# Kernel tuning notes

Hardware: AMD Instinct MI355X
Metric: run time of the kernel (lower is better)

Reference implementation:

```python
import jax, jax.numpy as jnp
import numpy as np

N = 100000
E = 1600000
D_IN = 64
D_H = 64
D_OUT = 10
G = 512
EPS = 1e-5


def setup_inputs() -> dict:
    key = jax.random.key(0)
    ks = jax.random.split(key, 12)
    x = jax.random.normal(ks[0], (N, D_IN), dtype=jnp.float32)
    edge_index = jax.random.randint(ks[1], (2, E), 0, N, dtype=jnp.int64)
    batch = jnp.sort(jax.random.randint(ks[2], (N,), 0, G, dtype=jnp.int64))

    def glorot(k, fan_in, fan_out):
        lim = float(np.sqrt(6.0 / (fan_in + fan_out)))
        return jax.random.uniform(k, (fan_in, fan_out), jnp.float32, -lim, lim)

    params = {
        'W1': glorot(ks[3], D_IN, D_H), 'b1': jnp.zeros((D_H,), jnp.float32),
        'g1': jnp.ones((D_H,), jnp.float32), 'be1': jnp.zeros((D_H,), jnp.float32),
        'W2': glorot(ks[4], D_H, D_H), 'b2': jnp.zeros((D_H,), jnp.float32),
        'g2': jnp.ones((D_H,), jnp.float32), 'be2': jnp.zeros((D_H,), jnp.float32),
        'W3': glorot(ks[5], D_H, D_H), 'b3': jnp.zeros((D_H,), jnp.float32),
        'g3': jnp.ones((D_H,), jnp.float32), 'be3': jnp.zeros((D_H,), jnp.float32),
        'Wfc': glorot(ks[6], D_H, D_OUT), 'bfc': jnp.zeros((D_OUT,), jnp.float32),
    }
    return dict(x=x, edge_index=edge_index, batch=batch, **params)


def _gcn_prep(edge_index):
    # add self-loops, compute symmetric degree normalization (PyG GCNConv)
    loop = jnp.arange(N, dtype=edge_index.dtype)
    src = jnp.concatenate([edge_index[0], loop])  # [E+N]
    dst = jnp.concatenate([edge_index[1], loop])
    deg = jax.ops.segment_sum(jnp.ones_like(dst, dtype=jnp.float32), dst, num_segments=N)
    dinv = jnp.where(deg > 0, jax.lax.rsqrt(deg), 0.0)
    norm = dinv[src] * dinv[dst]  # [E+N]
    return src, dst, norm


def _gcn_conv(x, src, dst, norm, W, b):
    h = x @ W                                   # [N, D]
    msg = h[src] * norm[:, None]                # gather + scale [E+N, D]
    out = jax.ops.segment_sum(msg, dst, num_segments=N)  # scatter-add
    return out + b


def _bn_relu(x, gamma, beta):
    # BatchNorm1d with batch statistics (training mode, biased variance)
    mu = jnp.mean(x, axis=0)
    var = jnp.mean(jnp.square(x - mu), axis=0)
    y = (x - mu) * jax.lax.rsqrt(var + EPS) * gamma + beta
    return jax.nn.relu(y)


def reference(x, edge_index, batch, W1, b1, g1, be1, W2, b2, g2, be2,
              W3, b3, g3, be3, Wfc, bfc):
    src, dst, norm = _gcn_prep(edge_index)
    # dropout treated as identity (eval-mode) for deterministic reference
    h = _bn_relu(_gcn_conv(x, src, dst, norm, W1, b1), g1, be1)
    h = _bn_relu(_gcn_conv(h, src, dst, norm, W2, b2), g2, be2)
    h = _bn_relu(_gcn_conv(h, src, dst, norm, W3, b3), g3, be3)
    # global mean pool over graphs
    sums = jax.ops.segment_sum(h, batch, num_segments=G)       # [G, D]
    cnt = jax.ops.segment_sum(jnp.ones((N,), jnp.float32), batch, num_segments=G)
    pooled = sums / jnp.maximum(cnt, 1.0)[:, None]
    return pooled @ Wfc + bfc  # [G, D_OUT]
```

## Files before the change

kernel.cpp:

```cpp
#include <hip/hip_runtime.h>

#define NNODES 100000
#define NEDGES 1600000
#define DH 64
#define NG 512
#define DOUT 10
#define EPSV 1e-5f
#define SCAN_BLKS 391
#define PCH 128

typedef short bf16x8 __attribute__((ext_vector_type(8)));
typedef float f32x4 __attribute__((ext_vector_type(4)));

__device__ inline unsigned bf16_rne(float x) {
    unsigned u = __float_as_uint(x);
    return (u + 0x7fffu + ((u >> 16) & 1u)) >> 16;
}
__device__ inline float bflo(unsigned u) { return __uint_as_float(u << 16); }
__device__ inline float bfhi(unsigned u) { return __uint_as_float(u & 0xffff0000u); }

__global__ void k_zero(int* __restrict__ cntdeg, float* __restrict__ pooled,
                       int* __restrict__ gstart, int* __restrict__ gend,
                       float* __restrict__ stats) {
    int i = blockIdx.x * 256 + threadIdx.x;
    if (i < NNODES) cntdeg[i] = 0;
    if (i < NG * DH) pooled[i] = 0.0f;
    if (i < NG) { gstart[i] = 0; gend[i] = 0; }
    if (i < 384) stats[i] = 0.0f;
}

__global__ void k_count(const int* __restrict__ dstE, int* __restrict__ cntdeg) {
    int e2 = blockIdx.x * 256 + threadIdx.x;
    if (e2 * 2 + 1 < NEDGES) {
        int2 d = ((const int2*)dstE)[e2];
        atomicAdd(&cntdeg[d.x], 1);
        atomicAdd(&cntdeg[d.y], 1);
    } else if (e2 * 2 < NEDGES) {
        atomicAdd(&cntdeg[dstE[e2 * 2]], 1);
    }
}

__global__ void k_scan1(const int* __restrict__ cntdeg, int* __restrict__ bsum,
                        float* __restrict__ dinv, const int* __restrict__ batch,
                        int* __restrict__ gstart, int* __restrict__ gend) {
    __shared__ int ls[256];
    int t = threadIdx.x, i = blockIdx.x * 256 + t;
    int v = (i < NNODES) ? cntdeg[i] : 0;
    if (i < NNODES) {
        dinv[i] = rsqrtf(1.0f + (float)v);
        int g = batch[i];
        if (i == 0 || batch[i - 1] != g) gstart[g] = i;
        if (i == NNODES - 1 || batch[i + 1] != g) gend[g] = i + 1;
    }
    ls[t] = v;
    __syncthreads();
#pragma unroll
    for (int off = 128; off > 0; off >>= 1) {
        if (t < off) ls[t] += ls[t + off];
        __syncthreads();
    }
    if (t == 0) bsum[blockIdx.x] = ls[0];
}

__global__ void __launch_bounds__(512) k_scan2(const int* __restrict__ bsum,
                                               int* __restrict__ boff) {
    __shared__ int ps[512];
    int t = threadIdx.x;
    int v = (t < SCAN_BLKS) ? bsum[t] : 0;
    ps[t] = v;
    __syncthreads();
#pragma unroll
    for (int off = 1; off < 512; off <<= 1) {
        int u = (t >= off) ? ps[t - off] : 0;
        __syncthreads();
        ps[t] += u;
        __syncthreads();
    }
    if (t < SCAN_BLKS) boff[t] = ps[t] - v;
}

__global__ void k_scan3(const int* __restrict__ cntdeg, const int* __restrict__ boff,
                        int* __restrict__ rowptr, int* __restrict__ cursor) {
    __shared__ int ps[256];
    int t = threadIdx.x, i = blockIdx.x * 256 + t;
    int v = (i < NNODES) ? cntdeg[i] : 0;
    ps[t] = v;
    __syncthreads();
#pragma unroll
    for (int off = 1; off < 256; off <<= 1) {
        int u = (t >= off) ? ps[t - off] : 0;
        __syncthreads();
        ps[t] += u;
        __syncthreads();
    }
    if (i < NNODES) {
        int ex = boff[blockIdx.x] + ps[t] - v;
        rowptr[i] = ex;
        cursor[i] = ex;
    }
    if (i == 0) rowptr[NNODES] = NEDGES;
}

__global__ void k_fill(const int* __restrict__ srcE, const int* __restrict__ dstE,
                       const float* __restrict__ dinv, int* __restrict__ cursor,
                       int2* __restrict__ csr) {
    int e = blockIdx.x * 256 + threadIdx.x;
    if (e >= NEDGES) return;
    int s = srcE[e], d = dstE[e];
    int pos = atomicAdd(&cursor[d], 1);
    float nm = dinv[s] * dinv[d];
    csr[pos] = make_int2(s, __float_as_int(nm));
}

__global__ void k_wprep(const float* __restrict__ W0, const float* __restrict__ W1,
                        const float* __restrict__ W2, short* __restrict__ wf) {
    int t = blockIdx.x * 256 + threadIdx.x;
    if (t >= 1536) return;
    int layer = t >> 9;
    int rem = t & 511;
    int ct = rem >> 7, ks = (rem >> 6) & 1, lane = rem & 63;
    const float* W = (layer == 0) ? W0 : (layer == 1) ? W1 : W2;
    short* hi = wf + layer * 8192 + rem * 8;
    short* lo = hi + 4096;
#pragma unroll
    for (int i = 0; i < 8; ++i) {
        int k = ks * 32 + ((lane >> 4) << 3) + i;
        int n = ct * 16 + (lane & 15);
        float v = W[k * 64 + n];
        unsigned h = bf16_rne(v);
        float fh = __uint_as_float(h << 16);
        unsigned l = bf16_rne(v - fh);
        hi[i] = (short)h;
        lo[i] = (short)l;
    }
}

template <int AFFINE>
__global__ void __launch_bounds__(256) k_mgemm(const float* __restrict__ in,
        const short* __restrict__ wf, const float* __restrict__ scale,
        const float* __restrict__ shift, unsigned short* __restrict__ out) {
    const int tid = threadIdx.x;
    const int wv = tid >> 6, l = tid & 63;
    const int r0 = blockIdx.x * 64 + wv * 16;
    const int row = r0 + (l & 15);
    const int kq = (l >> 4) << 3;

    float a[2][8];
    if (row < NNODES) {
        const float* rp = in + (size_t)row * 64 + kq;
        *(float4*)&a[0][0] = *(const float4*)(rp);
        *(float4*)&a[0][4] = *(const float4*)(rp + 4);
        *(float4*)&a[1][0] = *(const float4*)(rp + 32);
        *(float4*)&a[1][4] = *(const float4*)(rp + 36);
    } else {
#pragma unroll
        for (int ks = 0; ks < 2; ++ks)
#pragma unroll
            for (int i = 0; i < 8; ++i) a[ks][i] = 0.0f;
    }
    if (AFFINE) {
#pragma unroll
        for (int ks = 0; ks < 2; ++ks) {
            float4 sc0 = *(const float4*)(scale + kq + ks * 32);
            float4 sc1 = *(const float4*)(scale + kq + ks * 32 + 4);
            float4 sh0 = *(const float4*)(shift + kq + ks * 32);
            float4 sh1 = *(const float4*)(shift + kq + ks * 32 + 4);
            a[ks][0] = fmaxf(fmaf(a[ks][0], sc0.x, sh0.x), 0.0f);
            a[ks][1] = fmaxf(fmaf(a[ks][1], sc0.y, sh0.y), 0.0f);
            a[ks][2] = fmaxf(fmaf(a[ks][2], sc0.z, sh0.z), 0.0f);
            a[ks][3] = fmaxf(fmaf(a[ks][3], sc0.w, sh0.w), 0.0f);
            a[ks][4] = fmaxf(fmaf(a[ks][4], sc1.x, sh1.x), 0.0f);
            a[ks][5] = fmaxf(fmaf(a[ks][5], sc1.y, sh1.y), 0.0f);
            a[ks][6] = fmaxf(fmaf(a[ks][6], sc1.z, sh1.z), 0.0f);
            a[ks][7] = fmaxf(fmaf(a[ks][7], sc1.w, sh1.w), 0.0f);
        }
    }

    bf16x8 ah[2], al[2];
#pragma unroll
    for (int ks = 0; ks < 2; ++ks)
#pragma unroll
        for (int i = 0; i < 8; ++i) {
            unsigned h = bf16_rne(a[ks][i]);
            float fh = __uint_as_float(h << 16);
            ah[ks][i] = (short)h;
            al[ks][i] = (short)bf16_rne(a[ks][i] - fh);
        }

    const int rb = r0 + ((l >> 4) << 2);
    const int cb = l & 15;
#pragma unroll
    for (int ct = 0; ct < 4; ++ct) {
        const short* base = wf + (ct * 128 + l) * 8;
        bf16x8 wh0 = *(const bf16x8*)(base);
        bf16x8 wh1 = *(const bf16x8*)(base + 64 * 8);
        bf16x8 wl0 = *(const bf16x8*)(base + 4096);
        bf16x8 wl1 = *(const bf16x8*)(base + 4096 + 64 * 8);
        f32x4 acc = {0.0f, 0.0f, 0.0f, 0.0f};
        acc = __builtin_amdgcn_mfma_f32_16x16x32_bf16(ah[0], wh0, acc, 0, 0, 0);
        acc = __builtin_amdgcn_mfma_f32_16x16x32_bf16(ah[1], wh1, acc, 0, 0, 0);
        acc = __builtin_amdgcn_mfma_f32_16x16x32_bf16(al[0], wh0, acc, 0, 0, 0);
        acc = __builtin_amdgcn_mfma_f32_16x16x32_bf16(al[1], wh1, acc, 0, 0, 0);
        acc = __builtin_amdgcn_mfma_f32_16x16x32_bf16(ah[0], wl0, acc, 0, 0, 0);
        acc = __builtin_amdgcn_mfma_f32_16x16x32_bf16(ah[1], wl1, acc, 0, 0, 0);
        int n = ct * 16 + cb;
#pragma unroll
        for (int r = 0; r < 4; ++r)
            if (rb + r < NNODES) out[(size_t)(rb + r) * 64 + n] = (unsigned short)bf16_rne(acc[r]);
    }
}

__global__ void k_gather(const uint4* __restrict__ h, const int2* __restrict__ csr,
                         const int* __restrict__ rowptr, const float* __restrict__ dinv,
                         const float* __restrict__ bias, float* __restrict__ agg) {
    int t = blockIdx.x * 256 + threadIdx.x;
    int i = t >> 3, q = t & 7;
    if (i >= NNODES) return;
    float dv = dinv[i];
    float sn = dv * dv;
    float4 b0 = ((const float4*)bias)[q * 2];
    float4 b1 = ((const float4*)bias)[q * 2 + 1];
    uint4 hv = h[(size_t)i * 8 + q];
    float A[8], B[8];
    A[0] = fmaf(bflo(hv.x), sn, b0.x); A[1] = fmaf(bfhi(hv.x), sn, b0.y);
    A[2] = fmaf(bflo(hv.y), sn, b0.z); A[3] = fmaf(bfhi(hv.y), sn, b0.w);
    A[4] = fmaf(bflo(hv.z), sn, b1.x); A[5] = fmaf(bfhi(hv.z), sn, b1.y);
    A[6] = fmaf(bflo(hv.w), sn, b1.z); A[7] = fmaf(bfhi(hv.w), sn, b1.w);
#pragma unroll
    for (int k = 0; k < 8; ++k) B[k] = 0.0f;

    int e0 = rowptr[i], e1 = rowptr[i + 1];
    int e = e0;
    for (; e + 4 <= e1; e += 4) {
        int2 ea = csr[e], eb = csr[e + 1], ec = csr[e + 2], ed = csr[e + 3];
        float na = __int_as_float(ea.y), nb = __int_as_float(eb.y);
        float nc = __int_as_float(ec.y), nd = __int_as_float(ed.y);
        uint4 va = h[(size_t)ea.x * 8 + q];
        uint4 vb = h[(size_t)eb.x * 8 + q];
        uint4 vc = h[(size_t)ec.x * 8 + q];
        uint4 vd = h[(size_t)ed.x * 8 + q];
        A[0] = fmaf(bflo(va.x), na, A[0]); A[1] = fmaf(bfhi(va.x), na, A[1]);
        A[2] = fmaf(bflo(va.y), na, A[2]); A[3] = fmaf(bfhi(va.y), na, A[3]);
        A[4] = fmaf(bflo(va.z), na, A[4]); A[5] = fmaf(bfhi(va.z), na, A[5]);
        A[6] = fmaf(bflo(va.w), na, A[6]); A[7] = fmaf(bfhi(va.w), na, A[7]);
        B[0] = fmaf(bflo(vb.x), nb, B[0]); B[1] = fmaf(bfhi(vb.x), nb, B[1]);
        B[2] = fmaf(bflo(vb.y), nb, B[2]); B[3] = fmaf(bfhi(vb.y), nb, B[3]);
        B[4] = fmaf(bflo(vb.z), nb, B[4]); B[5] = fmaf(bfhi(vb.z), nb, B[5]);
        B[6] = fmaf(bflo(vb.w), nb, B[6]); B[7] = fmaf(bfhi(vb.w), nb, B[7]);
        A[0] = fmaf(bflo(vc.x), nc, A[0]); A[1] = fmaf(bfhi(vc.x), nc, A[1]);
        A[2] = fmaf(bflo(vc.y), nc, A[2]); A[3] = fmaf(bfhi(vc.y), nc, A[3]);
        A[4] = fmaf(bflo(vc.z), nc, A[4]); A[5] = fmaf(bfhi(vc.z), nc, A[5]);
        A[6] = fmaf(bflo(vc.w), nc, A[6]); A[7] = fmaf(bfhi(vc.w), nc, A[7]);
        B[0] = fmaf(bflo(vd.x), nd, B[0]); B[1] = fmaf(bfhi(vd.x), nd, B[1]);
        B[2] = fmaf(bflo(vd.y), nd, B[2]); B[3] = fmaf(bfhi(vd.y), nd, B[3]);
        B[4] = fmaf(bflo(vd.z), nd, B[4]); B[5] = fmaf(bfhi(vd.z), nd, B[5]);
        B[6] = fmaf(bflo(vd.w), nd, B[6]); B[7] = fmaf(bfhi(vd.w), nd, B[7]);
    }
    for (; e + 2 <= e1; e += 2) {
        int2 ea = csr[e], eb = csr[e + 1];
        float na = __int_as_float(ea.y), nb = __int_as_float(eb.y);
        uint4 va = h[(size_t)ea.x * 8 + q];
        uint4 vb = h[(size_t)eb.x * 8 + q];
        A[0] = fmaf(bflo(va.x), na, A[0]); A[1] = fmaf(bfhi(va.x), na, A[1]);
        A[2] = fmaf(bflo(va.y), na, A[2]); A[3] = fmaf(bfhi(va.y), na, A[3]);
        A[4] = fmaf(bflo(va.z), na, A[4]); A[5] = fmaf(bfhi(va.z), na, A[5]);
        A[6] = fmaf(bflo(va.w), na, A[6]); A[7] = fmaf(bfhi(va.w), na, A[7]);
        B[0] = fmaf(bflo(vb.x), nb, B[0]); B[1] = fmaf(bfhi(vb.x), nb, B[1]);
        B[2] = fmaf(bflo(vb.y), nb, B[2]); B[3] = fmaf(bfhi(vb.y), nb, B[3]);
        B[4] = fmaf(bflo(vb.z), nb, B[4]); B[5] = fmaf(bfhi(vb.z), nb, B[5]);
        B[6] = fmaf(bflo(vb.w), nb, B[6]); B[7] = fmaf(bfhi(vb.w), nb, B[7]);
    }
    if (e < e1) {
        int2 ea = csr[e];
        float na = __int_as_float(ea.y);
        uint4 va = h[(size_t)ea.x * 8 + q];
        A[0] = fmaf(bflo(va.x), na, A[0]); A[1] = fmaf(bfhi(va.x), na, A[1]);
        A[2] = fmaf(bflo(va.y), na, A[2]); A[3] = fmaf(bfhi(va.y), na, A[3]);
        A[4] = fmaf(bflo(va.z), na, A[4]); A[5] = fmaf(bfhi(va.z), na, A[5]);
        A[6] = fmaf(bflo(va.w), na, A[6]); A[7] = fmaf(bfhi(va.w), na, A[7]);
    }
    float4 r0, r1;
    r0.x = A[0] + B[0]; r0.y = A[1] + B[1]; r0.z = A[2] + B[2]; r0.w = A[3] + B[3];
    r1.x = A[4] + B[4]; r1.y = A[5] + B[5]; r1.z = A[6] + B[6]; r1.w = A[7] + B[7];
    ((float4*)agg)[(size_t)i * 16 + q * 2] = r0;
    ((float4*)agg)[(size_t)i * 16 + q * 2 + 1] = r1;
}

__global__ void k_stats(const float* __restrict__ agg, float* __restrict__ stats) {
    const int c = threadIdx.x & 63;
    float s = 0.f, ss = 0.f;
    for (int r = blockIdx.x * 4 + (threadIdx.x >> 6); r < NNODES; r += gridDim.x * 4) {
        float v = agg[(size_t)r * 64 + c];
        s += v;
        ss = fmaf(v, v, ss);
    }
    __shared__ float ls[256], lss[256];
    ls[threadIdx.x] = s;
    lss[threadIdx.x] = ss;
    __syncthreads();
    if (threadIdx.x < 64) {
        s = ls[c] + ls[c + 64] + ls[c + 128] + ls[c + 192];
        ss = lss[c] + lss[c + 64] + lss[c + 128] + lss[c + 192];
        unsafeAtomicAdd(&stats[c], s);
        unsafeAtomicAdd(&stats[64 + c], ss);
    }
}

__global__ void k_bnparams(const float* __restrict__ stats, const float* __restrict__ g,
                           const float* __restrict__ be, float* __restrict__ scale,
                           float* __restrict__ shift) {
    int c = threadIdx.x;
    if (c < 64) {
        float mu = stats[c] * (1.0f / NNODES);
        float var = stats[64 + c] * (1.0f / NNODES) - mu * mu;
        float sc = g[c] * rsqrtf(var + EPSV);
        scale[c] = sc;
        shift[c] = fmaf(-mu, sc, be[c]);
    }
}

__global__ void k_pool(const float* __restrict__ agg, const float* __restrict__ scale,
                       const float* __restrict__ shift, const int* __restrict__ batch,
                       float* __restrict__ pooled) {
    const int tid = threadIdx.x;
    const int c = tid & 63, r = tid >> 6;
    const int i0 = blockIdx.x * PCH;
    const float sc = scale[c], sh = shift[c];
    float acc = 0.0f;
    int cur = -1;
#pragma unroll 4
    for (int k = 0; k < PCH / 4; ++k) {
        int i = i0 + k * 4 + r;
        if (i >= NNODES) break;
        int g = batch[i];
        if (g != cur) {
            if (cur >= 0) unsafeAtomicAdd(&pooled[cur * 64 + c], acc);
            acc = 0.0f;
            cur = g;
        }
        acc += fmaxf(fmaf(agg[(size_t)i * 64 + c], sc, sh), 0.0f);
    }
    if (cur >= 0) unsafeAtomicAdd(&pooled[cur * 64 + c], acc);
}

__global__ void k_final(const float* __restrict__ pooled, const int* __restrict__ gstart,
                        const int* __restrict__ gend, const float* __restrict__ Wfc,
                        const float* __restrict__ bfc, float* __restrict__ out) {
    __shared__ float p[64];
    __shared__ float ic;
    int g = blockIdx.x, tid = threadIdx.x;
    p[tid] = pooled[(size_t)g * 64 + tid];
    if (tid == 0) ic = 1.0f / fmaxf((float)(gend[g] - gstart[g]), 1.0f);
    __syncthreads();
    if (tid < DOUT) {
        float a = bfc[tid];
#pragma unroll 8
        for (int c = 0; c < 64; ++c) a = fmaf(p[c] * ic, Wfc[c * DOUT + tid], a);
        out[g * DOUT + tid] = a;
    }
}

extern "C" void kernel_launch(void* const* d_in, const int* in_sizes, int n_in,
                              void* d_out, int out_size, void* d_ws, size_t ws_size,
                              hipStream_t stream) {
    const float* x = (const float*)d_in[0];
    const int* ei = (const int*)d_in[1];
    const int* batch = (const int*)d_in[2];
    const int* srcE = ei;
    const int* dstE = ei + NEDGES;
    const float* W[3] = {(const float*)d_in[3], (const float*)d_in[7], (const float*)d_in[11]};
    const float* B[3] = {(const float*)d_in[4], (const float*)d_in[8], (const float*)d_in[12]};
    const float* Gm[3] = {(const float*)d_in[5], (const float*)d_in[9], (const float*)d_in[13]};
    const float* Be[3] = {(const float*)d_in[6], (const float*)d_in[10], (const float*)d_in[14]};
    const float* Wfc = (const float*)d_in[15];
    const float* bfc = (const float*)d_in[16];
    float* out = (float*)d_out;

    float* f = (float*)d_ws;
    float* dinv = f;
    int* cntdeg = (int*)(f + 100000);
    int* rowptr = (int*)(f + 200000);
    int* cursor = (int*)(f + 300016);
    int2* csr = (int2*)(f + 400016);
    unsigned short* h = (unsigned short*)(f + 3600016);
    float* agg = f + 3600016 + 3200000;
    float* stats = agg + (size_t)NNODES * DH;
    float* scale = stats + 384;
    float* shift = scale + 64;
    float* pooled = shift + 64;
    int* gstart = (int*)(pooled + NG * DH);
    int* gend = gstart + NG;
    short* wf = (short*)(gend + NG);
    int* bsum = (int*)((short*)wf + 24576);
    int* boff = bsum + 400;

    k_zero<<<(NNODES + 255) / 256, 256, 0, stream>>>(cntdeg, pooled, gstart, gend, stats);
    k_count<<<(NEDGES / 2 + 255) / 256, 256, 0, stream>>>(dstE, cntdeg);
    k_scan1<<<SCAN_BLKS, 256, 0, stream>>>(cntdeg, bsum, dinv, batch, gstart, gend);
    k_scan2<<<1, 512, 0, stream>>>(bsum, boff);
    k_scan3<<<SCAN_BLKS, 256, 0, stream>>>(cntdeg, boff, rowptr, cursor);
    k_fill<<<(NEDGES + 255) / 256, 256, 0, stream>>>(srcE, dstE, dinv, cursor, csr);
    k_wprep<<<6, 256, 0, stream>>>(W[0], W[1], W[2], wf);

    const int gemm_grid = (NNODES + 63) / 64;
    for (int l = 0; l < 3; ++l) {
        const float* in = (l == 0) ? x : agg;
        if (l == 0)
            k_mgemm<0><<<gemm_grid, 256, 0, stream>>>(in, wf + l * 8192, scale, shift, h);
        else
            k_mgemm<1><<<gemm_grid, 256, 0, stream>>>(in, wf + l * 8192, scale, shift, h);
        k_gather<<<(NNODES * 8 + 255) / 256, 256, 0, stream>>>((const uint4*)h, csr, rowptr, dinv, B[l], agg);
        k_stats<<<512, 256, 0, stream>>>(agg, stats + l * 128);
        k_bnparams<<<1, 64, 0, stream>>>(stats + l * 128, Gm[l], Be[l], scale, shift);
    }

    k_pool<<<(NNODES + PCH - 1) / PCH, 256, 0, stream>>>(agg, scale, shift, batch, pooled);
    k_final<<<NG, 64, 0, stream>>>(pooled, gstart, gend, Wfc, bfc, out);
}
```

Before: 549.6 us.

## Store only source indices in CSR and factor dst normalization out of gather

The CSR now holds only the 4-byte source index instead of an (index, norm) pair. The gather applies the source-side dinv through a random load of dinv[src] and multiplies the destination-side dinv once after accumulation, which halves the CSR stream bandwidth and the fill-kernel writes. The trade is an extra scattered dinv load per edge, though that 400KB array should stay cache resident. Separately, the stats kernel now reads float4 vectors, with 16 row groups per block and a wider shared-memory reduction.

```diff
diff --git a/kernel.cpp b/kernel.cpp
--- a/kernel.cpp
+++ b/kernel.cpp
@@ -102,14 +102,12 @@
 }
 
 __global__ void k_fill(const int* __restrict__ srcE, const int* __restrict__ dstE,
-                       const float* __restrict__ dinv, int* __restrict__ cursor,
-                       int2* __restrict__ csr) {
+                       int* __restrict__ cursor, int* __restrict__ csr4) {
     int e = blockIdx.x * 256 + threadIdx.x;
     if (e >= NEDGES) return;
     int s = srcE[e], d = dstE[e];
     int pos = atomicAdd(&cursor[d], 1);
-    float nm = dinv[s] * dinv[d];
-    csr[pos] = make_int2(s, __float_as_int(nm));
+    csr4[pos] = s;
 }
 
 __global__ void k_wprep(const float* __restrict__ W0, const float* __restrict__ W1,
@@ -210,35 +208,31 @@
     }
 }
 
-__global__ void k_gather(const uint4* __restrict__ h, const int2* __restrict__ csr,
+__global__ void k_gather(const uint4* __restrict__ h, const int* __restrict__ csr4,
                          const int* __restrict__ rowptr, const float* __restrict__ dinv,
                          const float* __restrict__ bias, float* __restrict__ agg) {
     int t = blockIdx.x * 256 + threadIdx.x;
     int i = t >> 3, q = t & 7;
     if (i >= NNODES) return;
     float dv = dinv[i];
-    float sn = dv * dv;
-    float4 b0 = ((const float4*)bias)[q * 2];
-    float4 b1 = ((const float4*)bias)[q * 2 + 1];
     uint4 hv = h[(size_t)i * 8 + q];
     float A[8], B[8];
-    A[0] = fmaf(bflo(hv.x), sn, b0.x); A[1] = fmaf(bfhi(hv.x), sn, b0.y);
-    A[2] = fmaf(bflo(hv.y), sn, b0.z); A[3] = fmaf(bfhi(hv.y), sn, b0.w);
-    A[4] = fmaf(bflo(hv.z), sn, b1.x); A[5] = fmaf(bfhi(hv.z), sn, b1.y);
-    A[6] = fmaf(bflo(hv.w), sn, b1.z); A[7] = fmaf(bfhi(hv.w), sn, b1.w);
+    A[0] = bflo(hv.x) * dv; A[1] = bfhi(hv.x) * dv;
+    A[2] = bflo(hv.y) * dv; A[3] = bfhi(hv.y) * dv;
+    A[4] = bflo(hv.z) * dv; A[5] = bfhi(hv.z) * dv;
+    A[6] = bflo(hv.w) * dv; A[7] = bfhi(hv.w) * dv;
 #pragma unroll
     for (int k = 0; k < 8; ++k) B[k] = 0.0f;
 
     int e0 = rowptr[i], e1 = rowptr[i + 1];
     int e = e0;
     for (; e + 4 <= e1; e += 4) {
-        int2 ea = csr[e], eb = csr[e + 1], ec = csr[e + 2], ed = csr[e + 3];
-        float na = __int_as_float(ea.y), nb = __int_as_float(eb.y);
-        float nc = __int_as_float(ec.y), nd = __int_as_float(ed.y);
-        uint4 va = h[(size_t)ea.x * 8 + q];
-        uint4 vb = h[(size_t)eb.x * 8 + q];
-        uint4 vc = h[(size_t)ec.x * 8 + q];
-        uint4 vd = h[(size_t)ed.x * 8 + q];
+        int sa = csr4[e], sb = csr4[e + 1], sc = csr4[e + 2], sd = csr4[e + 3];
+        float na = dinv[sa], nb = dinv[sb], nc = dinv[sc], nd = dinv[sd];
+        uint4 va = h[(size_t)sa * 8 + q];
+        uint4 vb = h[(size_t)sb * 8 + q];
+        uint4 vc = h[(size_t)sc * 8 + q];
+        uint4 vd = h[(size_t)sd * 8 + q];
         A[0] = fmaf(bflo(va.x), na, A[0]); A[1] = fmaf(bfhi(va.x), na, A[1]);
         A[2] = fmaf(bflo(va.y), na, A[2]); A[3] = fmaf(bfhi(va.y), na, A[3]);
         A[4] = fmaf(bflo(va.z), na, A[4]); A[5] = fmaf(bfhi(va.z), na, A[5]);
@@ -257,10 +251,10 @@
         B[6] = fmaf(bflo(vd.w), nd, B[6]); B[7] = fmaf(bfhi(vd.w), nd, B[7]);
     }
     for (; e + 2 <= e1; e += 2) {
-        int2 ea = csr[e], eb = csr[e + 1];
-        float na = __int_as_float(ea.y), nb = __int_as_float(eb.y);
-        uint4 va = h[(size_t)ea.x * 8 + q];
-        uint4 vb = h[(size_t)eb.x * 8 + q];
+        int sa = csr4[e], sb = csr4[e + 1];
+        float na = dinv[sa], nb = dinv[sb];
+        uint4 va = h[(size_t)sa * 8 + q];
+        uint4 vb = h[(size_t)sb * 8 + q];
         A[0] = fmaf(bflo(va.x), na, A[0]); A[1] = fmaf(bfhi(va.x), na, A[1]);
         A[2] = fmaf(bflo(va.y), na, A[2]); A[3] = fmaf(bfhi(va.y), na, A[3]);
         A[4] = fmaf(bflo(va.z), na, A[4]); A[5] = fmaf(bfhi(va.z), na, A[5]);
@@ -271,38 +265,52 @@
         B[6] = fmaf(bflo(vb.w), nb, B[6]); B[7] = fmaf(bfhi(vb.w), nb, B[7]);
     }
     if (e < e1) {
-        int2 ea = csr[e];
-        float na = __int_as_float(ea.y);
-        uint4 va = h[(size_t)ea.x * 8 + q];
+        int sa = csr4[e];
+        float na = dinv[sa];
+        uint4 va = h[(size_t)sa * 8 + q];
         A[0] = fmaf(bflo(va.x), na, A[0]); A[1] = fmaf(bfhi(va.x), na, A[1]);
         A[2] = fmaf(bflo(va.y), na, A[2]); A[3] = fmaf(bfhi(va.y), na, A[3]);
         A[4] = fmaf(bflo(va.z), na, A[4]); A[5] = fmaf(bfhi(va.z), na, A[5]);
         A[6] = fmaf(bflo(va.w), na, A[6]); A[7] = fmaf(bfhi(va.w), na, A[7]);
     }
+    float4 b0 = ((const float4*)bias)[q * 2];
+    float4 b1 = ((const float4*)bias)[q * 2 + 1];
     float4 r0, r1;
-    r0.x = A[0] + B[0]; r0.y = A[1] + B[1]; r0.z = A[2] + B[2]; r0.w = A[3] + B[3];
-    r1.x = A[4] + B[4]; r1.y = A[5] + B[5]; r1.z = A[6] + B[6]; r1.w = A[7] + B[7];
+    r0.x = fmaf(A[0] + B[0], dv, b0.x); r0.y = fmaf(A[1] + B[1], dv, b0.y);
+    r0.z = fmaf(A[2] + B[2], dv, b0.z); r0.w = fmaf(A[3] + B[3], dv, b0.w);
+    r1.x = fmaf(A[4] + B[4], dv, b1.x); r1.y = fmaf(A[5] + B[5], dv, b1.y);
+    r1.z = fmaf(A[6] + B[6], dv, b1.z); r1.w = fmaf(A[7] + B[7], dv, b1.w);
     ((float4*)agg)[(size_t)i * 16 + q * 2] = r0;
     ((float4*)agg)[(size_t)i * 16 + q * 2 + 1] = r1;
 }
 
 __global__ void k_stats(const float* __restrict__ agg, float* __restrict__ stats) {
-    const int c = threadIdx.x & 63;
-    float s = 0.f, ss = 0.f;
-    for (int r = blockIdx.x * 4 + (threadIdx.x >> 6); r < NNODES; r += gridDim.x * 4) {
-        float v = agg[(size_t)r * 64 + c];
-        s += v;
-        ss = fmaf(v, v, ss);
-    }
-    __shared__ float ls[256], lss[256];
-    ls[threadIdx.x] = s;
-    lss[threadIdx.x] = ss;
+    const int tid = threadIdx.x;
+    const int c4 = (tid & 15) * 4;
+    const int rg = tid >> 4;
+    float s0 = 0, s1 = 0, s2 = 0, s3 = 0;
+    float q0 = 0, q1 = 0, q2 = 0, q3 = 0;
+    for (int r = blockIdx.x * 16 + rg; r < NNODES; r += gridDim.x * 16) {
+        float4 v = *(const float4*)(agg + (size_t)r * 64 + c4);
+        s0 += v.x; s1 += v.y; s2 += v.z; s3 += v.w;
+        q0 = fmaf(v.x, v.x, q0); q1 = fmaf(v.y, v.y, q1);
+        q2 = fmaf(v.z, v.z, q2); q3 = fmaf(v.w, v.w, q3);
+    }
+    __shared__ float ls[16 * 64], lq[16 * 64];
+    ls[rg * 64 + c4 + 0] = s0; ls[rg * 64 + c4 + 1] = s1;
+    ls[rg * 64 + c4 + 2] = s2; ls[rg * 64 + c4 + 3] = s3;
+    lq[rg * 64 + c4 + 0] = q0; lq[rg * 64 + c4 + 1] = q1;
+    lq[rg * 64 + c4 + 2] = q2; lq[rg * 64 + c4 + 3] = q3;
     __syncthreads();
-    if (threadIdx.x < 64) {
-        s = ls[c] + ls[c + 64] + ls[c + 128] + ls[c + 192];
-        ss = lss[c] + lss[c + 64] + lss[c + 128] + lss[c + 192];
-        unsafeAtomicAdd(&stats[c], s);
-        unsafeAtomicAdd(&stats[64 + c], ss);
+    if (tid < 64) {
+        float s = 0, q = 0;
+#pragma unroll
+        for (int g = 0; g < 16; ++g) {
+            s += ls[g * 64 + tid];
+            q += lq[g * 64 + tid];
+        }
+        unsafeAtomicAdd(&stats[tid], s);
+        unsafeAtomicAdd(&stats[64 + tid], q);
     }
 }
 
@@ -381,9 +389,9 @@
     int* cntdeg = (int*)(f + 100000);
     int* rowptr = (int*)(f + 200000);
     int* cursor = (int*)(f + 300016);
-    int2* csr = (int2*)(f + 400016);
-    unsigned short* h = (unsigned short*)(f + 3600016);
-    float* agg = f + 3600016 + 3200000;
+    int* csr4 = (int*)(f + 400016);
+    unsigned short* h = (unsigned short*)(f + 2000016);
+    float* agg = f + 5200016;
     float* stats = agg + (size_t)NNODES * DH;
     float* scale = stats + 384;
     float* shift = scale + 64;
@@ -399,7 +407,7 @@
     k_scan1<<<SCAN_BLKS, 256, 0, stream>>>(cntdeg, bsum, dinv, batch, gstart, gend);
     k_scan2<<<1, 512, 0, stream>>>(bsum, boff);
     k_scan3<<<SCAN_BLKS, 256, 0, stream>>>(cntdeg, boff, rowptr, cursor);
-    k_fill<<<(NEDGES + 255) / 256, 256, 0, stream>>>(srcE, dstE, dinv, cursor, csr);
+    k_fill<<<(NEDGES + 255) / 256, 256, 0, stream>>>(srcE, dstE, cursor, csr4);
     k_wprep<<<6, 256, 0, stream>>>(W[0], W[1], W[2], wf);
 
     const int gemm_grid = (NNODES + 63) / 64;
@@ -409,7 +417,7 @@
             k_mgemm<0><<<gemm_grid, 256, 0, stream>>>(in, wf + l * 8192, scale, shift, h);
         else
             k_mgemm<1><<<gemm_grid, 256, 0, stream>>>(in, wf + l * 8192, scale, shift, h);
-        k_gather<<<(NNODES * 8 + 255) / 256, 256, 0, stream>>>((const uint4*)h, csr, rowptr, dinv, B[l], agg);
+        k_gather<<<(NNODES * 8 + 255) / 256, 256, 0, stream>>>((const uint4*)h, csr4, rowptr, dinv, B[l], agg);
         k_stats<<<512, 256, 0, stream>>>(agg, stats + l * 128);
         k_bnparams<<<1, 64, 0, stream>>>(stats + l * 128, Gm[l], Be[l], scale, shift);
     }
```

Result: slower. 569.8 us (+3.7%).
